# Kernel optimization log

Hardware: AMD Instinct MI355X
Metric: run time of the kernel (lower is better)

Reference implementation:

```python
import jax, jax.numpy as jnp
import numpy as np

CLAMP = 1e-4


def setup_inputs() -> dict:
    key = jax.random.key(0)
    k1, k2 = jax.random.split(key)
    B, C, H, W = 8, 21, 512, 512
    pred = jax.random.normal(k1, (B, C, H, W), dtype=jnp.float32)
    # valid labels are 1..C-1 (0 = background skipped; class C never appears,
    # matching the original code's loop-with-skip behavior)
    label = jax.random.randint(k2, (B, H, W), 1, C, dtype=jnp.int32)
    return {"pred": pred, "label": label}


def _lovasz(pred, label):
    num_classes = pred.shape[1]
    # [B,C,H,W] -> [N, C], sigmoid + clamp
    p = jnp.transpose(pred, (0, 2, 3, 1)).reshape(-1, num_classes)
    p = jnp.clip(jax.nn.sigmoid(p.astype(jnp.float32)), CLAMP, 1.0 - CLAMP)
    lab = label.reshape(-1)

    # classes 1..num_classes-1 (class num_classes is never present in labels,
    # so its iteration in the original loop always hits `continue`)
    classes = jnp.arange(1, num_classes)
    masks = (lab[None, :] == classes[:, None]).astype(jnp.float32)  # [C-1, N]
    preds_c = p[:, 1:num_classes].T                                  # [C-1, N]

    errors = jnp.abs(masks - preds_c)                                # [C-1, N]
    order = jnp.argsort(-errors, axis=1)                             # descending
    errors_sorted = jnp.take_along_axis(errors, order, axis=1)
    masks_sorted = jnp.take_along_axis(masks, order, axis=1)

    # lovasz_grad, vectorized over classes
    gts = jnp.sum(masks_sorted, axis=1, keepdims=True)               # [C-1, 1]
    intersection = gts - jnp.cumsum(masks_sorted, axis=1)
    union = gts + jnp.cumsum(1.0 - masks_sorted, axis=1)
    jac = 1.0 - intersection / union
    jac = jnp.concatenate([jac[:, :1], jac[:, 1:] - jac[:, :-1]], axis=1)

    per_class = jnp.sum(errors_sorted * jac, axis=1)                 # [C-1]
    present = gts[:, 0] > 0
    count = jnp.sum(present.astype(jnp.float32))
    return jnp.sum(jnp.where(present, per_class, 0.0)) / count


def reference(pred, label):
    return _lovasz(pred, label)
```

## Files before the change

kernel.cpp:

```cpp
#include <hip/hip_runtime.h>

#define NBINS  128
#define NCLS   20
#define CDIM   21
#define HW     (512 * 512)
#define NPIX   (8 * HW)
#define NCHUNK 512
#define CHUNK  (NPIX / NCHUNK)
#define NCOPY  8
#define XSCALE 10.6666667f
#define XBIAS  64.0f

__device__ __forceinline__ float4 gld_f4(const float* p) {
    float4 r;
    asm volatile("global_load_dwordx4 %0, %1, off" : "=v"(r) : "v"(p));
    return r;
}
__device__ __forceinline__ int4 gld_i4(const int* p) {
    int4 r;
    asm volatile("global_load_dwordx4 %0, %1, off" : "=v"(r) : "v"(p));
    return r;
}

__global__ __launch_bounds__(256) void zero_ws(unsigned* __restrict__ w, int n) {
    int i = blockIdx.x * 256 + threadIdx.x;
    if (i < n) w[i] = 0u;
}

__global__ __launch_bounds__(256, 4) void lovasz_hist(const float* __restrict__ pred,
                                                      const int* __restrict__ label,
                                                      unsigned long long* __restrict__ g_hist) {
    __shared__ unsigned s_hist[NCLS * NBINS];
    const int tid = threadIdx.x;

    const long base = (long)blockIdx.x * CHUNK;
    const int  b    = (int)(base / HW);
    const long hw0  = base - (long)b * HW;
    const float* pbase = pred + ((long)b * CDIM + 1) * HW + hw0 + tid * 4;
    const int*   q     = label + base + tid * 4;

    int4 l[4];
#pragma unroll
    for (int t = 0; t < 4; ++t) l[t] = gld_i4(q + t * 1024);
    float4 buf[3][5];
#pragma unroll
    for (int k = 0; k < 5; ++k) buf[0][k] = gld_f4(pbase + (long)k * HW);
#pragma unroll
    for (int k = 0; k < 5; ++k) buf[1][k] = gld_f4(pbase + (long)(5 + k) * HW);

    for (int i = tid; i < NCLS * NBINS; i += 256) s_hist[i] = 0u;
    __syncthreads();

    auto compute5 = [&](const float4* x, int cbase, const int4& lab) {
#pragma unroll
        for (int j = 0; j < 4; ++j) {
            const int lv = (j == 0) ? lab.x : (j == 1) ? lab.y : (j == 2) ? lab.z : lab.w;
#pragma unroll
            for (int k = 0; k < 5; ++k) {
                const float xv = (j == 0) ? x[k].x : (j == 1) ? x[k].y
                               : (j == 2) ? x[k].z : x[k].w;
                const bool  pos = (lv == cbase + k + 1);
                const float t   = pos ? -xv : xv;
                const float bf  = fminf(fmaxf(__builtin_fmaf(t, XSCALE, XBIAS), 0.0f), 127.0f);
                const int   bin = (int)bf;
                atomicAdd(&s_hist[(cbase + k) * NBINS + bin], pos ? 0x10001u : 1u);
            }
        }
    };

#pragma unroll
    for (int g = 0; g < 16; ++g) {
        if (g + 2 < 16) {
            const int gg = g + 2;
#pragma unroll
            for (int k = 0; k < 5; ++k)
                buf[gg % 3][k] =
                    gld_f4(pbase + (long)((gg & 3) * 5 + k) * HW + (gg >> 2) * 1024);
        }
        if (g < 14)       asm volatile("s_waitcnt vmcnt(10)" ::: "memory");
        else if (g == 14) asm volatile("s_waitcnt vmcnt(5)" ::: "memory");
        else              asm volatile("s_waitcnt vmcnt(0)" ::: "memory");
        __builtin_amdgcn_sched_barrier(0);
        compute5(buf[g % 3], (g & 3) * 5, l[g >> 2]);
    }

    __syncthreads();

    unsigned long long* gh = g_hist + (size_t)(blockIdx.x & (NCOPY - 1)) * (NCLS * NBINS);
    for (int i = tid; i < NCLS * NBINS; i += 256) {
        const unsigned v = s_hist[i];
        if (v) {
            const unsigned long long pk =
                (unsigned long long)(v & 0xFFFFu) | ((unsigned long long)(v >> 16) << 32);
            atomicAdd(&gh[i], pk);
        }
    }
}

__global__ __launch_bounds__(1024) void lovasz_scan(const unsigned long long* __restrict__ g_hist,
                                                    float* __restrict__ out) {
    __shared__ float cls_sum[NCLS];
    __shared__ float cls_cnt[NCLS];
    const int wid  = threadIdx.x >> 6;
    const int lane = threadIdx.x & 63;

#pragma unroll
    for (int it = 0; it < 2; ++it) {
        const int cls = it * 16 + wid;
        if (cls < NCLS) {
            const int bin_lo = 126 - 2 * lane;
            int vc0 = 0, vp0 = 0, vc1 = 0, vp1 = 0;
#pragma unroll
            for (int r = 0; r < NCOPY; ++r) {
                const ulonglong2 v = *reinterpret_cast<const ulonglong2*>(
                    g_hist + ((size_t)r * NCLS + cls) * NBINS + bin_lo);
                vc1 += (int)(v.x & 0xFFFFFFFFull); vp1 += (int)(v.x >> 32);
                vc0 += (int)(v.y & 0xFFFFFFFFull); vp0 += (int)(v.y >> 32);
            }
            const int sc = vc0 + vc1, sp = vp0 + vp1;
            int ic = sc, ip = sp;
#pragma unroll
            for (int d = 1; d < 64; d <<= 1) {
                const int tc = __shfl_up(ic, d, 64);
                const int tp = __shfl_up(ip, d, 64);
                if (lane >= d) { ic += tc; ip += tp; }
            }
            const int G   = __shfl(ip, 63, 64);
            const int ec0 = ic - sc, ep0 = ip - sp;
            float contrib = 0.0f;
            if (G > 0) {
                const float fG = (float)G;
                auto J = [&](int i, int m) {
                    return 1.0f - (fG - (float)m) / (fG + (float)(i - m));
                };
                auto EMID = [&](int bn) {
                    const float xm = ((float)bn + 0.5f) * (12.0f / (float)NBINS) - 6.0f;
                    return 1.0f / (1.0f + __expf(-xm));
                };
                if (vc0) {
                    contrib += EMID(127 - 2 * lane) *
                               (J(ec0 + vc0, ep0 + vp0) - J(ec0, ep0));
                }
                if (vc1) {
                    const int ec = ec0 + vc0, ep = ep0 + vp0;
                    contrib += EMID(126 - 2 * lane) *
                               (J(ec + vc1, ep + vp1) - J(ec, ep));
                }
            }
#pragma unroll
            for (int d = 32; d > 0; d >>= 1) contrib += __shfl_down(contrib, d, 64);
            if (lane == 0) {
                cls_sum[cls] = contrib;
                cls_cnt[cls] = (G > 0) ? 1.0f : 0.0f;
            }
        }
    }
    __syncthreads();
    if (threadIdx.x == 0) {
        float s = 0.0f, n = 0.0f;
        for (int c = 0; c < NCLS; ++c) { s += cls_sum[c]; n += cls_cnt[c]; }
        out[0] = s / n;
    }
}

extern "C" void kernel_launch(void* const* d_in, const int* in_sizes, int n_in,
                              void* d_out, int out_size, void* d_ws, size_t ws_size,
                              hipStream_t stream) {
    const float* pred  = (const float*)d_in[0];
    const int*   label = (const int*)d_in[1];

    unsigned long long* g_hist = (unsigned long long*)d_ws;
    float* out = (float*)d_out;

    const int nzero = NCOPY * NCLS * NBINS * 2;
    zero_ws<<<(nzero + 255) / 256, 256, 0, stream>>>((unsigned*)g_hist, nzero);
    lovasz_hist<<<NCHUNK, 256, 0, stream>>>(pred, label, g_hist);
    lovasz_scan<<<1, 1024, 0, stream>>>(g_hist, out);
}
```

Before: 41.18 us.

## Replace global atomic histogram merge with per-block partials and parallel per-class scan

Each histogram block now writes its full shared-memory histogram to its own slice of workspace instead of atomically adding packed 64-bit values into 8 replicated copies. This removes the zeroing kernel. A 20-block scan kernel then reduces the 512 partials per class, and a tiny final kernel averages over classes. The prefetch pipeline is also deepened from 3 to 4 buffers, with launch bounds relaxed to allow more registers. In exchange the scan now reads about 5 MB of partials, one more kernel is launched, and occupancy may drop.

```diff
diff --git a/kernel.cpp b/kernel.cpp
--- a/kernel.cpp
+++ b/kernel.cpp
@@ -7,7 +7,7 @@
 #define NPIX   (8 * HW)
 #define NCHUNK 512
 #define CHUNK  (NPIX / NCHUNK)
-#define NCOPY  8
+#define HSZ    (NCLS * NBINS)
 #define XSCALE 10.6666667f
 #define XBIAS  64.0f
 
@@ -22,15 +22,10 @@
     return r;
 }
 
-__global__ __launch_bounds__(256) void zero_ws(unsigned* __restrict__ w, int n) {
-    int i = blockIdx.x * 256 + threadIdx.x;
-    if (i < n) w[i] = 0u;
-}
-
-__global__ __launch_bounds__(256, 4) void lovasz_hist(const float* __restrict__ pred,
+__global__ __launch_bounds__(256, 2) void lovasz_hist(const float* __restrict__ pred,
                                                       const int* __restrict__ label,
-                                                      unsigned long long* __restrict__ g_hist) {
-    __shared__ unsigned s_hist[NCLS * NBINS];
+                                                      unsigned* __restrict__ g_part) {
+    __shared__ unsigned s_hist[HSZ];
     const int tid = threadIdx.x;
 
     const long base = (long)blockIdx.x * CHUNK;
@@ -42,13 +37,14 @@
     int4 l[4];
 #pragma unroll
     for (int t = 0; t < 4; ++t) l[t] = gld_i4(q + t * 1024);
-    float4 buf[3][5];
+    float4 buf[4][5];
 #pragma unroll
-    for (int k = 0; k < 5; ++k) buf[0][k] = gld_f4(pbase + (long)k * HW);
+    for (int gg = 0; gg < 3; ++gg)
 #pragma unroll
-    for (int k = 0; k < 5; ++k) buf[1][k] = gld_f4(pbase + (long)(5 + k) * HW);
+        for (int k = 0; k < 5; ++k)
+            buf[gg][k] = gld_f4(pbase + (long)(gg * 5 + k) * HW);
 
-    for (int i = tid; i < NCLS * NBINS; i += 256) s_hist[i] = 0u;
+    for (int i = tid; i < HSZ; i += 256) s_hist[i] = 0u;
     __syncthreads();
 
     auto compute5 = [&](const float4* x, int cbase, const int4& lab) {
@@ -70,97 +66,109 @@
 
 #pragma unroll
     for (int g = 0; g < 16; ++g) {
-        if (g + 2 < 16) {
-            const int gg = g + 2;
+        if (g + 3 < 16) {
+            const int gg = g + 3;
 #pragma unroll
             for (int k = 0; k < 5; ++k)
-                buf[gg % 3][k] =
+                buf[gg % 4][k] =
                     gld_f4(pbase + (long)((gg & 3) * 5 + k) * HW + (gg >> 2) * 1024);
         }
-        if (g < 14)       asm volatile("s_waitcnt vmcnt(10)" ::: "memory");
+        if (g < 13)       asm volatile("s_waitcnt vmcnt(15)" ::: "memory");
+        else if (g == 13) asm volatile("s_waitcnt vmcnt(10)" ::: "memory");
         else if (g == 14) asm volatile("s_waitcnt vmcnt(5)" ::: "memory");
         else              asm volatile("s_waitcnt vmcnt(0)" ::: "memory");
         __builtin_amdgcn_sched_barrier(0);
-        compute5(buf[g % 3], (g & 3) * 5, l[g >> 2]);
+        compute5(buf[g % 4], (g & 3) * 5, l[g >> 2]);
     }
 
     __syncthreads();
 
-    unsigned long long* gh = g_hist + (size_t)(blockIdx.x & (NCOPY - 1)) * (NCLS * NBINS);
-    for (int i = tid; i < NCLS * NBINS; i += 256) {
-        const unsigned v = s_hist[i];
-        if (v) {
-            const unsigned long long pk =
-                (unsigned long long)(v & 0xFFFFu) | ((unsigned long long)(v >> 16) << 32);
-            atomicAdd(&gh[i], pk);
+    unsigned* gp = g_part + (size_t)blockIdx.x * HSZ;
+#pragma unroll
+    for (int i = tid; i < HSZ; i += 256) gp[i] = s_hist[i];
+}
+
+__global__ __launch_bounds__(1024) void lovasz_scan(const unsigned* __restrict__ g_part,
+                                                    float* __restrict__ cls_out) {
+    const int c    = blockIdx.x;
+    const int tid  = threadIdx.x;
+    const int rch  = tid >> 7;
+    const int bin  = tid & 127;
+    const unsigned* gp = g_part + (size_t)c * NBINS + bin;
+
+    unsigned vc = 0, vp = 0;
+    const int r0 = rch * 64;
+#pragma unroll
+    for (int bt = 0; bt < 8; ++bt) {
+        unsigned pk = 0;
+#pragma unroll
+        for (int k = 0; k < 8; ++k)
+            pk += gp[(size_t)(r0 + bt * 8 + k) * HSZ];
+        vc += pk & 0xFFFFu;
+        vp += pk >> 16;
+    }
+    __shared__ unsigned s_c[8][128], s_p[8][128];
+    s_c[rch][bin] = vc;
+    s_p[rch][bin] = vp;
+    __syncthreads();
+
+    const int d    = tid;
+    const int bn   = 127 - d;
+    const int lane = tid & 63;
+    const int w    = tid >> 6;
+    int tc = 0, tp = 0;
+    if (tid < 128) {
+#pragma unroll
+        for (int r = 0; r < 8; ++r) { tc += s_c[r][bn]; tp += s_p[r][bn]; }
+    }
+    int ic = tc, ip = tp;
+#pragma unroll
+    for (int dd = 1; dd < 64; dd <<= 1) {
+        const int t0 = __shfl_up(ic, dd, 64);
+        const int t1 = __shfl_up(ip, dd, 64);
+        if (lane >= dd) { ic += t0; ip += t1; }
+    }
+    __shared__ int wc[2], wp[2];
+    __shared__ float wsum[2];
+    if (tid < 128 && lane == 63) { wc[w] = ic; wp[w] = ip; }
+    __syncthreads();
+
+    float contrib = 0.0f;
+    int G = 0;
+    if (tid < 128) {
+        G = wp[0] + wp[1];
+        if (w == 1) { ic += wc[0]; ip += wp[0]; }
+        const int ec = ic - tc, ep = ip - tp;
+        if (G > 0 && tc > 0) {
+            const float fG = (float)G;
+            auto J = [&](int i, int m) {
+                return 1.0f - (fG - (float)m) / (fG + (float)(i - m));
+            };
+            const float xm = ((float)bn + 0.5f) * (12.0f / (float)NBINS) - 6.0f;
+            const float em = 1.0f / (1.0f + __expf(-xm));
+            contrib = em * (J(ec + tc, ep + tp) - J(ec, ep));
         }
+    }
+#pragma unroll
+    for (int dd = 32; dd > 0; dd >>= 1) contrib += __shfl_down(contrib, dd, 64);
+    if (tid < 128 && lane == 0) wsum[w] = contrib;
+    __syncthreads();
+    if (tid == 0) {
+        cls_out[c * 2]     = wsum[0] + wsum[1];
+        cls_out[c * 2 + 1] = (G > 0) ? 1.0f : 0.0f;
     }
 }
 
-__global__ __launch_bounds__(1024) void lovasz_scan(const unsigned long long* __restrict__ g_hist,
-                                                    float* __restrict__ out) {
-    __shared__ float cls_sum[NCLS];
-    __shared__ float cls_cnt[NCLS];
-    const int wid  = threadIdx.x >> 6;
+__global__ void lovasz_final(const float* __restrict__ cls_out, float* __restrict__ out) {
     const int lane = threadIdx.x & 63;
-
+    float s = 0.0f, n = 0.0f;
+    if (lane < NCLS) { s = cls_out[lane * 2]; n = cls_out[lane * 2 + 1]; }
 #pragma unroll
-    for (int it = 0; it < 2; ++it) {
-        const int cls = it * 16 + wid;
-        if (cls < NCLS) {
-            const int bin_lo = 126 - 2 * lane;
-            int vc0 = 0, vp0 = 0, vc1 = 0, vp1 = 0;
-#pragma unroll
-            for (int r = 0; r < NCOPY; ++r) {
-                const ulonglong2 v = *reinterpret_cast<const ulonglong2*>(
-                    g_hist + ((size_t)r * NCLS + cls) * NBINS + bin_lo);
-                vc1 += (int)(v.x & 0xFFFFFFFFull); vp1 += (int)(v.x >> 32);
-                vc0 += (int)(v.y & 0xFFFFFFFFull); vp0 += (int)(v.y >> 32);
-            }
-            const int sc = vc0 + vc1, sp = vp0 + vp1;
-            int ic = sc, ip = sp;
-#pragma unroll
-            for (int d = 1; d < 64; d <<= 1) {
-                const int tc = __shfl_up(ic, d, 64);
-                const int tp = __shfl_up(ip, d, 64);
-                if (lane >= d) { ic += tc; ip += tp; }
-            }
-            const int G   = __shfl(ip, 63, 64);
-            const int ec0 = ic - sc, ep0 = ip - sp;
-            float contrib = 0.0f;
-            if (G > 0) {
-                const float fG = (float)G;
-                auto J = [&](int i, int m) {
-                    return 1.0f - (fG - (float)m) / (fG + (float)(i - m));
-                };
-                auto EMID = [&](int bn) {
-                    const float xm = ((float)bn + 0.5f) * (12.0f / (float)NBINS) - 6.0f;
-                    return 1.0f / (1.0f + __expf(-xm));
-                };
-                if (vc0) {
-                    contrib += EMID(127 - 2 * lane) *
-                               (J(ec0 + vc0, ep0 + vp0) - J(ec0, ep0));
-                }
-                if (vc1) {
-                    const int ec = ec0 + vc0, ep = ep0 + vp0;
-                    contrib += EMID(126 - 2 * lane) *
-                               (J(ec + vc1, ep + vp1) - J(ec, ep));
-                }
-            }
-#pragma unroll
-            for (int d = 32; d > 0; d >>= 1) contrib += __shfl_down(contrib, d, 64);
-            if (lane == 0) {
-                cls_sum[cls] = contrib;
-                cls_cnt[cls] = (G > 0) ? 1.0f : 0.0f;
-            }
-        }
+    for (int dd = 32; dd > 0; dd >>= 1) {
+        s += __shfl_down(s, dd, 64);
+        n += __shfl_down(n, dd, 64);
     }
-    __syncthreads();
-    if (threadIdx.x == 0) {
-        float s = 0.0f, n = 0.0f;
-        for (int c = 0; c < NCLS; ++c) { s += cls_sum[c]; n += cls_cnt[c]; }
-        out[0] = s / n;
-    }
+    if (threadIdx.x == 0) out[0] = s / n;
 }
 
 extern "C" void kernel_launch(void* const* d_in, const int* in_sizes, int n_in,
@@ -169,11 +177,11 @@
     const float* pred  = (const float*)d_in[0];
     const int*   label = (const int*)d_in[1];
 
-    unsigned long long* g_hist = (unsigned long long*)d_ws;
-    float* out = (float*)d_out;
+    unsigned* g_part = (unsigned*)d_ws;
+    float*    cls_out = (float*)(g_part + (size_t)NCHUNK * HSZ);
+    float*    out     = (float*)d_out;
 
-    const int nzero = NCOPY * NCLS * NBINS * 2;
-    zero_ws<<<(nzero + 255) / 256, 256, 0, stream>>>((unsigned*)g_hist, nzero);
-    lovasz_hist<<<NCHUNK, 256, 0, stream>>>(pred, label, g_hist);
-    lovasz_scan<<<1, 1024, 0, stream>>>(g_hist, out);
+    lovasz_hist<<<NCHUNK, 256, 0, stream>>>(pred, label, g_part);
+    lovasz_scan<<<NCLS, 1024, 0, stream>>>(g_part, cls_out);
+    lovasz_final<<<1, 64, 0, stream>>>(cls_out, out);
 }
```

New measurement: 42.09 us. 1.02x slower.

## Replace global atomic histogram merge with per-block partials and a reduce kernel

Applied to the files above, without the earlier changes.

The histogram kernel now writes each block's full shared histogram to its own slice of workspace instead of doing 64-bit atomics into eight shared copies. A new reduce kernel sums the 512 partials per bin, which removes the zeroing kernel and the global atomic contention. The block size doubles to 512 threads, so each thread handles half as many pixel groups. The cost is about 5 MB of extra partial-histogram traffic and one more launch. Per-block bin counts must also stay within the 16-bit packed fields.

```diff
diff --git a/kernel.cpp b/kernel.cpp
--- a/kernel.cpp
+++ b/kernel.cpp
@@ -7,7 +7,7 @@
 #define NPIX   (8 * HW)
 #define NCHUNK 512
 #define CHUNK  (NPIX / NCHUNK)
-#define NCOPY  8
+#define HSZ    (NCLS * NBINS)
 #define XSCALE 10.6666667f
 #define XBIAS  64.0f
 
@@ -22,15 +22,10 @@
     return r;
 }
 
-__global__ __launch_bounds__(256) void zero_ws(unsigned* __restrict__ w, int n) {
-    int i = blockIdx.x * 256 + threadIdx.x;
-    if (i < n) w[i] = 0u;
-}
-
-__global__ __launch_bounds__(256, 4) void lovasz_hist(const float* __restrict__ pred,
+__global__ __launch_bounds__(512, 4) void lovasz_hist(const float* __restrict__ pred,
                                                       const int* __restrict__ label,
-                                                      unsigned long long* __restrict__ g_hist) {
-    __shared__ unsigned s_hist[NCLS * NBINS];
+                                                      unsigned* __restrict__ g_part) {
+    __shared__ unsigned s_hist[HSZ];
     const int tid = threadIdx.x;
 
     const long base = (long)blockIdx.x * CHUNK;
@@ -39,16 +34,17 @@
     const float* pbase = pred + ((long)b * CDIM + 1) * HW + hw0 + tid * 4;
     const int*   q     = label + base + tid * 4;
 
-    int4 l[4];
-#pragma unroll
-    for (int t = 0; t < 4; ++t) l[t] = gld_i4(q + t * 1024);
+    int4 l[2];
+    l[0] = gld_i4(q);
+    l[1] = gld_i4(q + 2048);
     float4 buf[3][5];
 #pragma unroll
-    for (int k = 0; k < 5; ++k) buf[0][k] = gld_f4(pbase + (long)k * HW);
+    for (int gg = 0; gg < 2; ++gg)
 #pragma unroll
-    for (int k = 0; k < 5; ++k) buf[1][k] = gld_f4(pbase + (long)(5 + k) * HW);
+        for (int k = 0; k < 5; ++k)
+            buf[gg][k] = gld_f4(pbase + (long)(gg * 5 + k) * HW);
 
-    for (int i = tid; i < NCLS * NBINS; i += 256) s_hist[i] = 0u;
+    for (int i = tid; i < HSZ; i += 512) s_hist[i] = 0u;
     __syncthreads();
 
     auto compute5 = [&](const float4* x, int cbase, const int4& lab) {
@@ -69,35 +65,57 @@
     };
 
 #pragma unroll
-    for (int g = 0; g < 16; ++g) {
-        if (g + 2 < 16) {
+    for (int g = 0; g < 8; ++g) {
+        if (g + 2 < 8) {
             const int gg = g + 2;
 #pragma unroll
             for (int k = 0; k < 5; ++k)
                 buf[gg % 3][k] =
-                    gld_f4(pbase + (long)((gg & 3) * 5 + k) * HW + (gg >> 2) * 1024);
+                    gld_f4(pbase + (long)((gg & 3) * 5 + k) * HW + (gg >> 2) * 2048);
         }
-        if (g < 14)       asm volatile("s_waitcnt vmcnt(10)" ::: "memory");
-        else if (g == 14) asm volatile("s_waitcnt vmcnt(5)" ::: "memory");
-        else              asm volatile("s_waitcnt vmcnt(0)" ::: "memory");
+        if (g < 6)       asm volatile("s_waitcnt vmcnt(10)" ::: "memory");
+        else if (g == 6) asm volatile("s_waitcnt vmcnt(5)" ::: "memory");
+        else             asm volatile("s_waitcnt vmcnt(0)" ::: "memory");
         __builtin_amdgcn_sched_barrier(0);
         compute5(buf[g % 3], (g & 3) * 5, l[g >> 2]);
     }
 
     __syncthreads();
 
-    unsigned long long* gh = g_hist + (size_t)(blockIdx.x & (NCOPY - 1)) * (NCLS * NBINS);
-    for (int i = tid; i < NCLS * NBINS; i += 256) {
-        const unsigned v = s_hist[i];
-        if (v) {
-            const unsigned long long pk =
-                (unsigned long long)(v & 0xFFFFu) | ((unsigned long long)(v >> 16) << 32);
-            atomicAdd(&gh[i], pk);
-        }
+    unsigned* gp = g_part + (size_t)blockIdx.x * HSZ;
+    for (int i = tid; i < HSZ; i += 512) gp[i] = s_hist[i];
+}
+
+__global__ __launch_bounds__(256) void lovasz_reduce(const unsigned* __restrict__ g_part,
+                                                     unsigned long long* __restrict__ H) {
+    const int t  = threadIdx.x;
+    const int i  = blockIdx.x * 16 + (t & 15);
+    const int rc = t >> 4;
+    const unsigned* gp = g_part + i;
+
+    unsigned vc = 0, vp = 0;
+#pragma unroll
+    for (int bt = 0; bt < 4; ++bt) {
+        unsigned pk = 0;
+#pragma unroll
+        for (int k = 0; k < 8; ++k)
+            pk += gp[(size_t)(rc * 32 + bt * 8 + k) * HSZ];
+        vc += pk & 0xFFFFu;
+        vp += pk >> 16;
+    }
+    __shared__ unsigned s_c[16][16], s_p[16][16];
+    s_c[rc][t & 15] = vc;
+    s_p[rc][t & 15] = vp;
+    __syncthreads();
+    if (t < 16) {
+        unsigned c = 0, p = 0;
+#pragma unroll
+        for (int r = 0; r < 16; ++r) { c += s_c[r][t]; p += s_p[r][t]; }
+        H[blockIdx.x * 16 + t] = (unsigned long long)c | ((unsigned long long)p << 32);
     }
 }
 
-__global__ __launch_bounds__(1024) void lovasz_scan(const unsigned long long* __restrict__ g_hist,
+__global__ __launch_bounds__(1024) void lovasz_scan(const unsigned long long* __restrict__ H,
                                                     float* __restrict__ out) {
     __shared__ float cls_sum[NCLS];
     __shared__ float cls_cnt[NCLS];
@@ -109,14 +127,9 @@
         const int cls = it * 16 + wid;
         if (cls < NCLS) {
             const int bin_lo = 126 - 2 * lane;
-            int vc0 = 0, vp0 = 0, vc1 = 0, vp1 = 0;
-#pragma unroll
-            for (int r = 0; r < NCOPY; ++r) {
-                const ulonglong2 v = *reinterpret_cast<const ulonglong2*>(
-                    g_hist + ((size_t)r * NCLS + cls) * NBINS + bin_lo);
-                vc1 += (int)(v.x & 0xFFFFFFFFull); vp1 += (int)(v.x >> 32);
-                vc0 += (int)(v.y & 0xFFFFFFFFull); vp0 += (int)(v.y >> 32);
-            }
+            const ulonglong2 v = *reinterpret_cast<const ulonglong2*>(H + cls * NBINS + bin_lo);
+            const int vc1 = (int)(v.x & 0xFFFFFFFFull), vp1 = (int)(v.x >> 32);
+            const int vc0 = (int)(v.y & 0xFFFFFFFFull), vp0 = (int)(v.y >> 32);
             const int sc = vc0 + vc1, sp = vp0 + vp1;
             int ic = sc, ip = sp;
 #pragma unroll
@@ -169,11 +182,11 @@
     const float* pred  = (const float*)d_in[0];
     const int*   label = (const int*)d_in[1];
 
-    unsigned long long* g_hist = (unsigned long long*)d_ws;
+    unsigned* g_part = (unsigned*)d_ws;
+    unsigned long long* H = (unsigned long long*)(g_part + (size_t)NCHUNK * HSZ);
     float* out = (float*)d_out;
 
-    const int nzero = NCOPY * NCLS * NBINS * 2;
-    zero_ws<<<(nzero + 255) / 256, 256, 0, stream>>>((unsigned*)g_hist, nzero);
-    lovasz_hist<<<NCHUNK, 256, 0, stream>>>(pred, label, g_hist);
-    lovasz_scan<<<1, 1024, 0, stream>>>(g_hist, out);
+    lovasz_hist<<<NCHUNK, 512, 0, stream>>>(pred, label, g_part);
+    lovasz_reduce<<<HSZ / 16, 256, 0, stream>>>(g_part, H);
+    lovasz_scan<<<1, 1024, 0, stream>>>(H, out);
 }
```

New measurement: 39.99 us (median of 2 runs). 1.03x faster.
